# Kernel tuning notes

Hardware: AMD Instinct MI355X
Metric: run time of the kernel (lower is better)

## Reference

```python
import jax, jax.numpy as jnp
import numpy as np

EPS = 1e-6
TEMPERATURE = 0.75
SINKHORN_ITERS = 7


def setup_inputs() -> dict:
    key = jax.random.key(0)
    ks = jax.random.split(key, 6)
    b, h, t, d_h = 4, 8, 4096, 64
    bs = 256
    nb = t // bs
    q = jax.random.normal(ks[0], (b, h, t, d_h), jnp.float32)
    k = jax.random.normal(ks[1], (b, h, t, d_h), jnp.float32)
    v = jax.random.normal(ks[2], (b, h, t, d_h), jnp.float32)
    # uniform noise for gumbel sampling in the sinkhorn sort net
    gumbel_u = jax.random.uniform(ks[3], (b * h, nb, nb), jnp.float32,
                                  minval=EPS, maxval=1.0 - EPS)
    W_out = jax.random.normal(ks[4], (2 * d_h, d_h), jnp.float32) / np.sqrt(2 * d_h)
    b_out = jnp.zeros((d_h,), jnp.float32)
    return {"q": q, "k": k, "v": v, "gumbel_u": gumbel_u,
            "W_out": W_out, "b_out": b_out, "bucket_size": bs}


def _sinkhorn(r, n_iters):
    # iterative row/col log-normalization of log-scores r: [bh, nb, nb]
    def body(r, _):
        r = r - jax.scipy.special.logsumexp(r, axis=2, keepdims=True)
        r = r - jax.scipy.special.logsumexp(r, axis=1, keepdims=True)
        return r, None
    r, _ = jax.lax.scan(body, r, None, length=n_iters)
    return jnp.exp(r)


def reference(q, k, v, gumbel_u, W_out, b_out, bucket_size):
    b, h, t, d_h = q.shape
    bh = b * h
    nb = t // bucket_size
    scale = d_h ** -0.5
    # merge batch/head and bucket: [bh, nb, bs, d_h]
    bq = q.reshape(bh, nb, bucket_size, d_h)
    bk = k.reshape(bh, nb, bucket_size, d_h)
    bv = v.reshape(bh, nb, bucket_size, d_h)
    # AttentionSortNet: bucket sums -> scores -> gumbel sinkhorn soft permutation
    q_sum = bq.sum(axis=2)  # [bh, nb, d_h]
    k_sum = bk.sum(axis=2)
    R0 = jax.nn.relu(jnp.einsum('bie,bje->bij', q_sum, k_sum) * scale)
    gumbel = -jnp.log(-jnp.log(gumbel_u + EPS) + EPS)
    r = (jnp.log(R0 + EPS) + gumbel) / TEMPERATURE
    R = _sinkhorn(r, SINKHORN_ITERS)  # [bh, nb, nb]
    # soft-reorder k/v buckets with R
    k_r = jnp.einsum('bij,bjsd->bisd', R, bk)
    v_r = jnp.einsum('bij,bjsd->bisd', R, bv)
    # local (within-bucket) attention
    local_s = jnp.einsum('bnie,bnje->bnij', bq, bk) * scale
    local_out = jnp.einsum('bnij,bnjd->bnid', jax.nn.softmax(local_s, axis=-1), bv)
    # attention over soft-sorted buckets
    sort_s = jnp.einsum('bnie,bnje->bnij', bq, k_r) * scale
    sort_out = jnp.einsum('bnij,bnjd->bnid', jax.nn.softmax(sort_s, axis=-1), v_r)
    # concat local + sorted heads, project 2*d_h -> d_h
    out = jnp.concatenate([local_out, sort_out], axis=-1)  # [bh, nb, bs, 2*d_h]
    out = out @ W_out + b_out
    return out.reshape(b, h, t, d_h)
```

## Files before the change

### kernel.cpp

```cpp
#include <hip/hip_runtime.h>
#include <math.h>


typedef __attribute__((ext_vector_type(8))) short short8;
typedef __attribute__((ext_vector_type(4))) float f32x4;

constexpr int BH = 32;
constexpr int NB = 16;
constexpr int BS = 256;
constexpr int D  = 64;
constexpr int BUCKET = BS * D;
constexpr float SCALE = 0.125f;

__device__ inline unsigned short bf16_rne(float x) {
  unsigned u = __builtin_bit_cast(unsigned, x);
  unsigned r = u + 0x7FFFu + ((u >> 16) & 1u);
  return (unsigned short)(r >> 16);
}
__device__ inline float bf16_to_f(unsigned short h) {
  unsigned u = ((unsigned)h) << 16;
  return __builtin_bit_cast(float, u);
}
__device__ inline void split2(float x, unsigned short& h, unsigned short& l) {
  h = bf16_rne(x);
  l = bf16_rne(x - bf16_to_f(h));
}
__device__ inline uint2 pack4(unsigned short a, unsigned short b,
                              unsigned short c, unsigned short d) {
  uint2 r;
  r.x = (unsigned)a | ((unsigned)b << 16);
  r.y = (unsigned)c | ((unsigned)d << 16);
  return r;
}

__global__ __launch_bounds__(256) void k_bucket_sums(
    const float* __restrict__ q, const float* __restrict__ k,
    float* __restrict__ qsum, float* __restrict__ ksum) {
  const int bid = blockIdx.x;
  const int t = threadIdx.x;
  const int d = t & 63;
  const int grp = t >> 6;
  const float* qb = q + (size_t)bid * BUCKET;
  const float* kb = k + (size_t)bid * BUCKET;
  float sq = 0.f, sk = 0.f;
  for (int s = grp; s < BS; s += 4) {
    sq += qb[s * D + d];
    sk += kb[s * D + d];
  }
  __shared__ float red[2][4][64];
  red[0][grp][d] = sq;
  red[1][grp][d] = sk;
  __syncthreads();
  if (t < 64) {
    qsum[bid * D + t] = red[0][0][t] + red[0][1][t] + red[0][2][t] + red[0][3][t];
  } else if (t < 128) {
    const int dd = t - 64;
    ksum[bid * D + dd] = red[1][0][dd] + red[1][1][dd] + red[1][2][dd] + red[1][3][dd];
  }
}

__global__ __launch_bounds__(256) void k_sinkhorn(
    const float* __restrict__ qsum, const float* __restrict__ ksum,
    const float* __restrict__ gu, float* __restrict__ R) {
  const int bh = blockIdx.x;
  const int t = threadIdx.x;
  const int i = t >> 4, j = t & 15;
  __shared__ float qs[16][64], ks[16][64], r[16][17];
  for (int idx = t; idx < NB * D; idx += 256) {
    qs[idx >> 6][idx & 63] = qsum[bh * NB * D + idx];
    ks[idx >> 6][idx & 63] = ksum[bh * NB * D + idx];
  }
  __syncthreads();
  float dot = 0.f;
  #pragma unroll
  for (int e = 0; e < D; ++e) dot += qs[i][e] * ks[j][e];
  const float R0 = fmaxf(dot * SCALE, 0.f);
  const float u = gu[bh * 256 + t];
  const float g = -logf(-logf(u + 1e-6f) + 1e-6f);
  float rv = (logf(R0 + 1e-6f) + g) * (1.0f / 0.75f);
  r[i][j] = rv;
  __syncthreads();
  for (int it = 0; it < 7; ++it) {
    float m = -1e30f;
    #pragma unroll
    for (int jj = 0; jj < 16; ++jj) m = fmaxf(m, r[i][jj]);
    float ssum = 0.f;
    #pragma unroll
    for (int jj = 0; jj < 16; ++jj) ssum += expf(r[i][jj] - m);
    float nv = r[i][j] - (m + logf(ssum));
    __syncthreads();
    r[i][j] = nv;
    __syncthreads();
    m = -1e30f;
    #pragma unroll
    for (int ii = 0; ii < 16; ++ii) m = fmaxf(m, r[ii][j]);
    ssum = 0.f;
    #pragma unroll
    for (int ii = 0; ii < 16; ++ii) ssum += expf(r[ii][j] - m);
    nv = r[i][j] - (m + logf(ssum));
    __syncthreads();
    r[i][j] = nv;
    __syncthreads();
  }
  R[bh * 256 + t] = expf(r[i][j]);
}

__global__ __launch_bounds__(256) void k_mix(
    const float* __restrict__ k, const float* __restrict__ v,
    const float* __restrict__ R,
    float* __restrict__ kr, float* __restrict__ vr) {
  const int bid = blockIdx.x;
  const int bh = bid >> 4;
  const int c4 = bid & 15;
  const int t = threadIdx.x;
  __shared__ float Rs[16][16];
  Rs[t >> 4][t & 15] = R[bh * 256 + t];
  __syncthreads();
  const int f = c4 * 256 + t;
  const float4* kb = (const float4*)(k + (size_t)bh * NB * BUCKET);
  const float4* vb = (const float4*)(v + (size_t)bh * NB * BUCKET);
  float4 ka[16], va[16];
  #pragma unroll
  for (int i = 0; i < 16; ++i) {
    ka[i] = make_float4(0.f, 0.f, 0.f, 0.f);
    va[i] = make_float4(0.f, 0.f, 0.f, 0.f);
  }
  #pragma unroll
  for (int j = 0; j < 16; ++j) {
    const float4 kv = kb[j * 4096 + f];
    const float4 vv = vb[j * 4096 + f];
    #pragma unroll
    for (int i = 0; i < 16; ++i) {
      const float w = Rs[i][j];
      ka[i].x += w * kv.x; ka[i].y += w * kv.y; ka[i].z += w * kv.z; ka[i].w += w * kv.w;
      va[i].x += w * vv.x; va[i].y += w * vv.y; va[i].z += w * vv.z; va[i].w += w * vv.w;
    }
  }
  float4* kro = (float4*)(kr + (size_t)bh * NB * BUCKET);
  float4* vro = (float4*)(vr + (size_t)bh * NB * BUCKET);
  #pragma unroll
  for (int i = 0; i < 16; ++i) {
    kro[i * 4096 + f] = ka[i];
    vro[i * 4096 + f] = va[i];
  }
}

__global__ __launch_bounds__(256, 2) void k_attn(
    const float* __restrict__ q,
    const float* __restrict__ k,  const float* __restrict__ v,
    const float* __restrict__ kr, const float* __restrict__ vr,
    const float* __restrict__ Wp, const float* __restrict__ bp,
    float* __restrict__ out) {
  const int bid = blockIdx.x;
  const int t = threadIdx.x;
  const int wv = t >> 6;
  const int lane = t & 63;
  const int g = lane >> 4;
  const int c = lane & 15;
  const size_t boff = (size_t)bid * BUCKET;

  __shared__ unsigned short Khi[32 * 72], Klo[32 * 72];
  __shared__ unsigned short VThi[64 * 40], VTlo[64 * 40];
  __shared__ float Plds[4][64 * 36];

  short8 Qhi[4][2], Qlo[4][2];
  #pragma unroll
  for (int qm = 0; qm < 4; ++qm) {
    #pragma unroll
    for (int ks = 0; ks < 2; ++ks) {
      const float* src = q + boff + (size_t)(64 * wv + 16 * qm + c) * D + 32 * ks + 8 * g;
      float4 a = *(const float4*)src;
      float4 b = *(const float4*)(src + 4);
      float xs[8] = {a.x, a.y, a.z, a.w, b.x, b.y, b.z, b.w};
      short8 hi, lo;
      #pragma unroll
      for (int e = 0; e < 8; ++e) {
        unsigned short h, l2;
        split2(xs[e] * SCALE, h, l2);
        hi[e] = (short)h; lo[e] = (short)l2;
      }
      Qhi[qm][ks] = hi; Qlo[qm][ks] = lo;
    }
  }
  short8 ONE8;
  #pragma unroll
  for (int e = 0; e < 8; ++e) ONE8[e] = (short)0x3F80;

  float* Pw = &Plds[wv][0];

  f32x4 Pacc[4][4];
  #pragma unroll
  for (int qm = 0; qm < 4; ++qm)
    #pragma unroll
    for (int dn = 0; dn < 4; ++dn) Pacc[qm][dn] = (f32x4){0.f, 0.f, 0.f, 0.f};

  #pragma unroll
  for (int pass = 0; pass < 2; ++pass) {
    const float* kb = (pass ? kr : k) + boff;
    const float* vb = (pass ? vr : v) + boff;
    f32x4 Oacc[4][4];
    f32x4 lacc[4];
    #pragma unroll
    for (int qm = 0; qm < 4; ++qm) {
      lacc[qm] = (f32x4){0.f, 0.f, 0.f, 0.f};
      #pragma unroll
      for (int dn = 0; dn < 4; ++dn) Oacc[qm][dn] = (f32x4){0.f, 0.f, 0.f, 0.f};
    }

    for (int p = 0; p < 8; ++p) {
      __syncthreads();
      if (t < 128) {
        #pragma unroll
        for (int i = 0; i < 4; ++i) {
          int cell = t + 128 * i;
          int kkr = cell >> 4, dq = cell & 15;
          float4 a = *(const float4*)(kb + (size_t)(32 * p + kkr) * D + 4 * dq);
          unsigned short h0, l0, h1, l1, h2, l2, h3, l3;
          split2(a.x, h0, l0); split2(a.y, h1, l1);
          split2(a.z, h2, l2); split2(a.w, h3, l3);
          *(uint2*)&Khi[kkr * 72 + 4 * dq] = pack4(h0, h1, h2, h3);
          *(uint2*)&Klo[kkr * 72 + 4 * dq] = pack4(l0, l1, l2, l3);
        }
      } else {
        int h2i = t - 128;
        int kkq = h2i >> 4, dq = h2i & 15;
        float4 rows[4];
        #pragma unroll
        for (int j = 0; j < 4; ++j)
          rows[j] = *(const float4*)(vb + (size_t)(32 * p + 4 * kkq + j) * D + 4 * dq);
        #pragma unroll
        for (int m = 0; m < 4; ++m) {
          float e0 = (m == 0) ? rows[0].x : (m == 1) ? rows[0].y : (m == 2) ? rows[0].z : rows[0].w;
          float e1 = (m == 0) ? rows[1].x : (m == 1) ? rows[1].y : (m == 2) ? rows[1].z : rows[1].w;
          float e2 = (m == 0) ? rows[2].x : (m == 1) ? rows[2].y : (m == 2) ? rows[2].z : rows[2].w;
          float e3 = (m == 0) ? rows[3].x : (m == 1) ? rows[3].y : (m == 2) ? rows[3].z : rows[3].w;
          unsigned short h0, l0, h1, l1, h2, l2, h3, l3;
          split2(e0, h0, l0); split2(e1, h1, l1);
          split2(e2, h2, l2); split2(e3, h3, l3);
          *(uint2*)&VThi[(4 * dq + m) * 40 + 4 * kkq] = pack4(h0, h1, h2, h3);
          *(uint2*)&VTlo[(4 * dq + m) * 40 + 4 * kkq] = pack4(l0, l1, l2, l3);
        }
      }
      __syncthreads();

      #pragma unroll
      for (int kn = 0; kn < 2; ++kn) {
        f32x4 S[4];
        #pragma unroll
        for (int qm = 0; qm < 4; ++qm) S[qm] = (f32x4){0.f, 0.f, 0.f, 0.f};
        #pragma unroll
        for (int ks = 0; ks < 2; ++ks) {
          short8 Bhi = *(const short8*)&Khi[(16 * kn + c) * 72 + 32 * ks + 8 * g];
          short8 Blo = *(const short8*)&Klo[(16 * kn + c) * 72 + 32 * ks + 8 * g];
          #pragma unroll
          for (int qm = 0; qm < 4; ++qm) {
            S[qm] = __builtin_amdgcn_mfma_f32_16x16x32_bf16(Qhi[qm][ks], Bhi, S[qm], 0, 0, 0);
            S[qm] = __builtin_amdgcn_mfma_f32_16x16x32_bf16(Qhi[qm][ks], Blo, S[qm], 0, 0, 0);
            S[qm] = __builtin_amdgcn_mfma_f32_16x16x32_bf16(Qlo[qm][ks], Bhi, S[qm], 0, 0, 0);
          }
        }
        #pragma unroll
        for (int qm = 0; qm < 4; ++qm)
          #pragma unroll
          for (int r = 0; r < 4; ++r)
            Pw[(16 * qm + 4 * g + r) * 36 + 16 * kn + c] = __expf(S[qm][r]);
      }

      short8 Phi[4], Plo[4];
      #pragma unroll
      for (int qm = 0; qm < 4; ++qm) {
        const float* pr = &Pw[(16 * qm + c) * 36 + 8 * g];
        f32x4 p0 = *(const f32x4*)pr;
        f32x4 p1 = *(const f32x4*)(pr + 4);
        float ps[8] = {p0[0], p0[1], p0[2], p0[3], p1[0], p1[1], p1[2], p1[3]};
        short8 hi, lo;
        #pragma unroll
        for (int e = 0; e < 8; ++e) {
          unsigned short h, l2;
          split2(ps[e], h, l2);
          hi[e] = (short)h; lo[e] = (short)l2;
        }
        Phi[qm] = hi; Plo[qm] = lo;
      }

      #pragma unroll
      for (int qm = 0; qm < 4; ++qm) {
        lacc[qm] = __builtin_amdgcn_mfma_f32_16x16x32_bf16(Phi[qm], ONE8, lacc[qm], 0, 0, 0);
        lacc[qm] = __builtin_amdgcn_mfma_f32_16x16x32_bf16(Plo[qm], ONE8, lacc[qm], 0, 0, 0);
      }

      #pragma unroll
      for (int dn = 0; dn < 4; ++dn) {
        short8 Vhi = *(const short8*)&VThi[(16 * dn + c) * 40 + 8 * g];
        short8 Vlo = *(const short8*)&VTlo[(16 * dn + c) * 40 + 8 * g];
        #pragma unroll
        for (int qm = 0; qm < 4; ++qm) {
          Oacc[qm][dn] = __builtin_amdgcn_mfma_f32_16x16x32_bf16(Phi[qm], Vhi, Oacc[qm][dn], 0, 0, 0);
          Oacc[qm][dn] = __builtin_amdgcn_mfma_f32_16x16x32_bf16(Phi[qm], Vlo, Oacc[qm][dn], 0, 0, 0);
          Oacc[qm][dn] = __builtin_amdgcn_mfma_f32_16x16x32_bf16(Plo[qm], Vhi, Oacc[qm][dn], 0, 0, 0);
        }
      }
    }

    f32x4 invs[4];
    #pragma unroll
    for (int qm = 0; qm < 4; ++qm)
      #pragma unroll
      for (int r = 0; r < 4; ++r) invs[qm][r] = 1.0f / lacc[qm][r];

    #pragma unroll
    for (int ks2 = 0; ks2 < 2; ++ks2) {
      #pragma unroll
      for (int qm = 0; qm < 4; ++qm)
        #pragma unroll
        for (int dnl = 0; dnl < 2; ++dnl) {
          const int dn = 2 * ks2 + dnl;
          #pragma unroll
          for (int r = 0; r < 4; ++r)
            Pw[(16 * qm + 4 * g + r) * 36 + 16 * dnl + c] = Oacc[qm][dn][r] * invs[qm][r];
        }
      short8 Ahi[4], Alo[4];
      #pragma unroll
      for (int qm = 0; qm < 4; ++qm) {
        const float* pr = &Pw[(16 * qm + c) * 36 + 8 * g];
        f32x4 p0 = *(const f32x4*)pr;
        f32x4 p1 = *(const f32x4*)(pr + 4);
        float ps[8] = {p0[0], p0[1], p0[2], p0[3], p1[0], p1[1], p1[2], p1[3]};
        short8 hi, lo;
        #pragma unroll
        for (int e = 0; e < 8; ++e) {
          unsigned short h, l2;
          split2(ps[e], h, l2);
          hi[e] = (short)h; lo[e] = (short)l2;
        }
        Ahi[qm] = hi; Alo[qm] = lo;
      }
      #pragma unroll
      for (int dn_o = 0; dn_o < 4; ++dn_o) {
        float wf[8];
        #pragma unroll
        for (int e = 0; e < 8; ++e)
          wf[e] = Wp[(size_t)(pass * 64 + 32 * ks2 + 8 * g + e) * 64 + 16 * dn_o + c];
        short8 WBhi, WBlo;
        #pragma unroll
        for (int e = 0; e < 8; ++e) {
          unsigned short h, l2;
          split2(wf[e], h, l2);
          WBhi[e] = (short)h; WBlo[e] = (short)l2;
        }
        #pragma unroll
        for (int qm = 0; qm < 4; ++qm) {
          Pacc[qm][dn_o] = __builtin_amdgcn_mfma_f32_16x16x32_bf16(Ahi[qm], WBhi, Pacc[qm][dn_o], 0, 0, 0);
          Pacc[qm][dn_o] = __builtin_amdgcn_mfma_f32_16x16x32_bf16(Ahi[qm], WBlo, Pacc[qm][dn_o], 0, 0, 0);
          Pacc[qm][dn_o] = __builtin_amdgcn_mfma_f32_16x16x32_bf16(Alo[qm], WBhi, Pacc[qm][dn_o], 0, 0, 0);
        }
      }
    }
  }

  float bvals[4];
  #pragma unroll
  for (int dn_o = 0; dn_o < 4; ++dn_o) bvals[dn_o] = bp[16 * dn_o + c];
  #pragma unroll
  for (int qm = 0; qm < 4; ++qm)
    #pragma unroll
    for (int dn_o = 0; dn_o < 4; ++dn_o)
      #pragma unroll
      for (int r = 0; r < 4; ++r) {
        const int row = 64 * wv + 16 * qm + 4 * g + r;
        out[((size_t)bid * 256 + row) * 64 + 16 * dn_o + c] = Pacc[qm][dn_o][r] + bvals[dn_o];
      }
}

extern "C" void kernel_launch(void* const* d_in, const int* in_sizes, int n_in,
                              void* d_out, int out_size, void* d_ws, size_t ws_size,
                              hipStream_t stream) {
  (void)in_sizes; (void)n_in; (void)out_size; (void)ws_size;
  const float* q  = (const float*)d_in[0];
  const float* k  = (const float*)d_in[1];
  const float* v  = (const float*)d_in[2];
  const float* gu = (const float*)d_in[3];
  const float* W  = (const float*)d_in[4];
  const float* b  = (const float*)d_in[5];
  float* out = (float*)d_out;

  float* ws   = (float*)d_ws;
  float* R    = ws;
  float* qsum = ws + 8192;
  float* ksum = qsum + 32768;
  float* kr   = ksum + 32768;
  float* vr   = kr + 8388608;

  hipLaunchKernelGGL(k_bucket_sums, dim3(BH * NB), dim3(256), 0, stream, q, k, qsum, ksum);
  hipLaunchKernelGGL(k_sinkhorn,    dim3(BH),      dim3(256), 0, stream, qsum, ksum, gu, R);
  hipLaunchKernelGGL(k_mix,         dim3(BH * NB), dim3(256), 0, stream, k, v, R, kr, vr);
  hipLaunchKernelGGL(k_attn,        dim3(BH * NB), dim3(256), 0, stream,
                     q, k, v, kr, vr, W, b, out);
}
```

Baseline: 283.4 us.

## Compute S transposed, keep P in registers, shrink LDS, raise occupancy

Several changes at once. The attention kernel computes S transposed (K as the A operand), so exponentiated scores stay in registers. Row sums come from register adds plus wave shuffles instead of MFMA-with-ones, and P and the normalized output are staged in LDS as packed bf16 hi/lo rather than fp32. The bf16 split is vectorized into pair packing, and the kernel's launch-bound occupancy target goes from 2 to 4. Separately, the bucket-sum kernel now uses float4 loads, and the mix kernel uses float2 with twice as many blocks and fewer registers. The risk is register spilling under the tighter launch bound and a slightly different summation order for the normalizer.

Result: slower. 513.7 us (+81.3%).

```diff
diff --git a/kernel.cpp b/kernel.cpp
--- a/kernel.cpp
+++ b/kernel.cpp
@@ -12,25 +12,18 @@
 constexpr int BUCKET = BS * D;
 constexpr float SCALE = 0.125f;
 
-__device__ inline unsigned short bf16_rne(float x) {
+__device__ inline unsigned bf16_rne_u(float x) {
   unsigned u = __builtin_bit_cast(unsigned, x);
-  unsigned r = u + 0x7FFFu + ((u >> 16) & 1u);
-  return (unsigned short)(r >> 16);
-}
-__device__ inline float bf16_to_f(unsigned short h) {
-  unsigned u = ((unsigned)h) << 16;
-  return __builtin_bit_cast(float, u);
-}
-__device__ inline void split2(float x, unsigned short& h, unsigned short& l) {
-  h = bf16_rne(x);
-  l = bf16_rne(x - bf16_to_f(h));
-}
-__device__ inline uint2 pack4(unsigned short a, unsigned short b,
-                              unsigned short c, unsigned short d) {
-  uint2 r;
-  r.x = (unsigned)a | ((unsigned)b << 16);
-  r.y = (unsigned)c | ((unsigned)d << 16);
-  return r;
+  return (u + 0x7FFFu + ((u >> 16) & 1u)) >> 16;
+}
+__device__ inline unsigned cvt2_bf16(float a, float b) {
+  return bf16_rne_u(a) | (bf16_rne_u(b) << 16);
+}
+__device__ inline void split_pair(float a, float b, unsigned& uhi, unsigned& ulo) {
+  uhi = cvt2_bf16(a, b);
+  float ha = __builtin_bit_cast(float, uhi << 16);
+  float hb = __builtin_bit_cast(float, uhi & 0xFFFF0000u);
+  ulo = cvt2_bf16(a - ha, b - hb);
 }
 
 __global__ __launch_bounds__(256) void k_bucket_sums(
@@ -38,24 +31,29 @@
     float* __restrict__ qsum, float* __restrict__ ksum) {
   const int bid = blockIdx.x;
   const int t = threadIdx.x;
-  const int d = t & 63;
-  const int grp = t >> 6;
-  const float* qb = q + (size_t)bid * BUCKET;
-  const float* kb = k + (size_t)bid * BUCKET;
-  float sq = 0.f, sk = 0.f;
-  for (int s = grp; s < BS; s += 4) {
-    sq += qb[s * D + d];
-    sk += kb[s * D + d];
-  }
-  __shared__ float red[2][4][64];
-  red[0][grp][d] = sq;
-  red[1][grp][d] = sk;
+  const int c4 = t & 15;
+  const int rg = t >> 4;
+  const float4* qb = (const float4*)(q + (size_t)bid * BUCKET);
+  const float4* kb = (const float4*)(k + (size_t)bid * BUCKET);
+  float4 sq = make_float4(0.f, 0.f, 0.f, 0.f);
+  float4 sk = make_float4(0.f, 0.f, 0.f, 0.f);
+  for (int s = rg; s < BS; s += 16) {
+    float4 a = qb[s * 16 + c4];
+    float4 b2 = kb[s * 16 + c4];
+    sq.x += a.x; sq.y += a.y; sq.z += a.z; sq.w += a.w;
+    sk.x += b2.x; sk.y += b2.y; sk.z += b2.z; sk.w += b2.w;
+  }
+  __shared__ float red[2][16][64];
+  *(float4*)&red[0][rg][4 * c4] = sq;
+  *(float4*)&red[1][rg][4 * c4] = sk;
   __syncthreads();
-  if (t < 64) {
-    qsum[bid * D + t] = red[0][0][t] + red[0][1][t] + red[0][2][t] + red[0][3][t];
-  } else if (t < 128) {
-    const int dd = t - 64;
-    ksum[bid * D + dd] = red[1][0][dd] + red[1][1][dd] + red[1][2][dd] + red[1][3][dd];
+  if (t < 128) {
+    const int which = t >> 6;
+    const int d = t & 63;
+    float s = 0.f;
+    #pragma unroll
+    for (int g2 = 0; g2 < 16; ++g2) s += red[which][g2][d];
+    (which ? ksum : qsum)[bid * D + d] = s;
   }
 }
 
@@ -105,47 +103,47 @@
   R[bh * 256 + t] = expf(r[i][j]);
 }
 
-__global__ __launch_bounds__(256) void k_mix(
+__global__ __launch_bounds__(256, 4) void k_mix(
     const float* __restrict__ k, const float* __restrict__ v,
     const float* __restrict__ R,
     float* __restrict__ kr, float* __restrict__ vr) {
   const int bid = blockIdx.x;
-  const int bh = bid >> 4;
-  const int c4 = bid & 15;
+  const int bh = bid >> 5;
+  const int ch = bid & 31;
   const int t = threadIdx.x;
   __shared__ float Rs[16][16];
   Rs[t >> 4][t & 15] = R[bh * 256 + t];
   __syncthreads();
-  const int f = c4 * 256 + t;
-  const float4* kb = (const float4*)(k + (size_t)bh * NB * BUCKET);
-  const float4* vb = (const float4*)(v + (size_t)bh * NB * BUCKET);
-  float4 ka[16], va[16];
+  const int f = ch * 256 + t;
+  const float2* kb = (const float2*)(k + (size_t)bh * NB * BUCKET);
+  const float2* vb = (const float2*)(v + (size_t)bh * NB * BUCKET);
+  float2 ka[16], va[16];
   #pragma unroll
   for (int i = 0; i < 16; ++i) {
-    ka[i] = make_float4(0.f, 0.f, 0.f, 0.f);
-    va[i] = make_float4(0.f, 0.f, 0.f, 0.f);
+    ka[i] = make_float2(0.f, 0.f);
+    va[i] = make_float2(0.f, 0.f);
   }
   #pragma unroll
   for (int j = 0; j < 16; ++j) {
-    const float4 kv = kb[j * 4096 + f];
-    const float4 vv = vb[j * 4096 + f];
+    const float2 kv = kb[j * 8192 + f];
+    const float2 vv = vb[j * 8192 + f];
     #pragma unroll
     for (int i = 0; i < 16; ++i) {
       const float w = Rs[i][j];
-      ka[i].x += w * kv.x; ka[i].y += w * kv.y; ka[i].z += w * kv.z; ka[i].w += w * kv.w;
-      va[i].x += w * vv.x; va[i].y += w * vv.y; va[i].z += w * vv.z; va[i].w += w * vv.w;
-    }
-  }
-  float4* kro = (float4*)(kr + (size_t)bh * NB * BUCKET);
-  float4* vro = (float4*)(vr + (size_t)bh * NB * BUCKET);
+      ka[i].x += w * kv.x; ka[i].y += w * kv.y;
+      va[i].x += w * vv.x; va[i].y += w * vv.y;
+    }
+  }
+  float2* kro = (float2*)(kr + (size_t)bh * NB * BUCKET);
+  float2* vro = (float2*)(vr + (size_t)bh * NB * BUCKET);
   #pragma unroll
   for (int i = 0; i < 16; ++i) {
-    kro[i * 4096 + f] = ka[i];
-    vro[i * 4096 + f] = va[i];
-  }
-}
-
-__global__ __launch_bounds__(256, 2) void k_attn(
+    kro[i * 8192 + f] = ka[i];
+    vro[i * 8192 + f] = va[i];
+  }
+}
+
+__global__ __launch_bounds__(256, 4) void k_attn(
     const float* __restrict__ q,
     const float* __restrict__ k,  const float* __restrict__ v,
     const float* __restrict__ kr, const float* __restrict__ vr,
@@ -161,7 +159,7 @@
 
   __shared__ unsigned short Khi[32 * 72], Klo[32 * 72];
   __shared__ unsigned short VThi[64 * 40], VTlo[64 * 40];
-  __shared__ float Plds[4][64 * 36];
+  __shared__ unsigned short Pbh[4][16 * 40], Pbl[4][16 * 40];
 
   short8 Qhi[4][2], Qlo[4][2];
   #pragma unroll
@@ -170,23 +168,21 @@
     for (int ks = 0; ks < 2; ++ks) {
       const float* src = q + boff + (size_t)(64 * wv + 16 * qm + c) * D + 32 * ks + 8 * g;
       float4 a = *(const float4*)src;
-      float4 b = *(const float4*)(src + 4);
-      float xs[8] = {a.x, a.y, a.z, a.w, b.x, b.y, b.z, b.w};
-      short8 hi, lo;
-      #pragma unroll
-      for (int e = 0; e < 8; ++e) {
-        unsigned short h, l2;
-        split2(xs[e] * SCALE, h, l2);
-        hi[e] = (short)h; lo[e] = (short)l2;
-      }
-      Qhi[qm][ks] = hi; Qlo[qm][ks] = lo;
-    }
-  }
-  short8 ONE8;
-  #pragma unroll
-  for (int e = 0; e < 8; ++e) ONE8[e] = (short)0x3F80;
-
-  float* Pw = &Plds[wv][0];
+      float4 b2 = *(const float4*)(src + 4);
+      unsigned h0, l0, h1, l1, h2, l2, h3, l3;
+      split_pair(a.x * SCALE, a.y * SCALE, h0, l0);
+      split_pair(a.z * SCALE, a.w * SCALE, h1, l1);
+      split_pair(b2.x * SCALE, b2.y * SCALE, h2, l2);
+      split_pair(b2.z * SCALE, b2.w * SCALE, h3, l3);
+      uint4 uh = make_uint4(h0, h1, h2, h3);
+      uint4 ul = make_uint4(l0, l1, l2, l3);
+      Qhi[qm][ks] = __builtin_bit_cast(short8, uh);
+      Qlo[qm][ks] = __builtin_bit_cast(short8, ul);
+    }
+  }
+
+  unsigned short* ph = Pbh[wv];
+  unsigned short* pl = Pbl[wv];
 
   f32x4 Pacc[4][4];
   #pragma unroll
@@ -199,10 +195,10 @@
     const float* kb = (pass ? kr : k) + boff;
     const float* vb = (pass ? vr : v) + boff;
     f32x4 Oacc[4][4];
-    f32x4 lacc[4];
+    float lrow[4];
     #pragma unroll
     for (int qm = 0; qm < 4; ++qm) {
-      lacc[qm] = (f32x4){0.f, 0.f, 0.f, 0.f};
+      lrow[qm] = 0.f;
       #pragma unroll
       for (int dn = 0; dn < 4; ++dn) Oacc[qm][dn] = (f32x4){0.f, 0.f, 0.f, 0.f};
     }
@@ -215,11 +211,11 @@
           int cell = t + 128 * i;
           int kkr = cell >> 4, dq = cell & 15;
           float4 a = *(const float4*)(kb + (size_t)(32 * p + kkr) * D + 4 * dq);
-          unsigned short h0, l0, h1, l1, h2, l2, h3, l3;
-          split2(a.x, h0, l0); split2(a.y, h1, l1);
-          split2(a.z, h2, l2); split2(a.w, h3, l3);
-          *(uint2*)&Khi[kkr * 72 + 4 * dq] = pack4(h0, h1, h2, h3);
-          *(uint2*)&Klo[kkr * 72 + 4 * dq] = pack4(l0, l1, l2, l3);
+          unsigned h0, l0, h1, l1;
+          split_pair(a.x, a.y, h0, l0);
+          split_pair(a.z, a.w, h1, l1);
+          *(uint2*)&Khi[kkr * 72 + 4 * dq] = make_uint2(h0, h1);
+          *(uint2*)&Klo[kkr * 72 + 4 * dq] = make_uint2(l0, l1);
         }
       } else {
         int h2i = t - 128;
@@ -234,59 +230,57 @@
           float e1 = (m == 0) ? rows[1].x : (m == 1) ? rows[1].y : (m == 2) ? rows[1].z : rows[1].w;
           float e2 = (m == 0) ? rows[2].x : (m == 1) ? rows[2].y : (m == 2) ? rows[2].z : rows[2].w;
           float e3 = (m == 0) ? rows[3].x : (m == 1) ? rows[3].y : (m == 2) ? rows[3].z : rows[3].w;
-          unsigned short h0, l0, h1, l1, h2, l2, h3, l3;
-          split2(e0, h0, l0); split2(e1, h1, l1);
-          split2(e2, h2, l2); split2(e3, h3, l3);
-          *(uint2*)&VThi[(4 * dq + m) * 40 + 4 * kkq] = pack4(h0, h1, h2, h3);
-          *(uint2*)&VTlo[(4 * dq + m) * 40 + 4 * kkq] = pack4(l0, l1, l2, l3);
+          unsigned h0, l0, h1, l1;
+          split_pair(e0, e1, h0, l0);
+          split_pair(e2, e3, h1, l1);
+          *(uint2*)&VThi[(4 * dq + m) * 40 + 4 * kkq] = make_uint2(h0, h1);
+          *(uint2*)&VTlo[(4 * dq + m) * 40 + 4 * kkq] = make_uint2(l0, l1);
         }
       }
       __syncthreads();
 
+      f32x4 pe[4][2];
       #pragma unroll
       for (int kn = 0; kn < 2; ++kn) {
-        f32x4 S[4];
-        #pragma unroll
-        for (int qm = 0; qm < 4; ++qm) S[qm] = (f32x4){0.f, 0.f, 0.f, 0.f};
+        f32x4 ST[4];
+        #pragma unroll
+        for (int qm = 0; qm < 4; ++qm) ST[qm] = (f32x4){0.f, 0.f, 0.f, 0.f};
         #pragma unroll
         for (int ks = 0; ks < 2; ++ks) {
-          short8 Bhi = *(const short8*)&Khi[(16 * kn + c) * 72 + 32 * ks + 8 * g];
-          short8 Blo = *(const short8*)&Klo[(16 * kn + c) * 72 + 32 * ks + 8 * g];
+          short8 KAhi = *(const short8*)&Khi[(16 * kn + c) * 72 + 32 * ks + 8 * g];
+          short8 KAlo = *(const short8*)&Klo[(16 * kn + c) * 72 + 32 * ks + 8 * g];
           #pragma unroll
           for (int qm = 0; qm < 4; ++qm) {
-            S[qm] = __builtin_amdgcn_mfma_f32_16x16x32_bf16(Qhi[qm][ks], Bhi, S[qm], 0, 0, 0);
-            S[qm] = __builtin_amdgcn_mfma_f32_16x16x32_bf16(Qhi[qm][ks], Blo, S[qm], 0, 0, 0);
-            S[qm] = __builtin_amdgcn_mfma_f32_16x16x32_bf16(Qlo[qm][ks], Bhi, S[qm], 0, 0, 0);
+            ST[qm] = __builtin_amdgcn_mfma_f32_16x16x32_bf16(KAhi, Qhi[qm][ks], ST[qm], 0, 0, 0);
+            ST[qm] = __builtin_amdgcn_mfma_f32_16x16x32_bf16(KAhi, Qlo[qm][ks], ST[qm], 0, 0, 0);
+            ST[qm] = __builtin_amdgcn_mfma_f32_16x16x32_bf16(KAlo, Qhi[qm][ks], ST[qm], 0, 0, 0);
           }
         }
         #pragma unroll
         for (int qm = 0; qm < 4; ++qm)
           #pragma unroll
-          for (int r = 0; r < 4; ++r)
-            Pw[(16 * qm + 4 * g + r) * 36 + 16 * kn + c] = __expf(S[qm][r]);
+          for (int r = 0; r < 4; ++r) pe[qm][kn][r] = __expf(ST[qm][r]);
+      }
+
+      #pragma unroll
+      for (int qm = 0; qm < 4; ++qm) {
+        lrow[qm] += ((pe[qm][0][0] + pe[qm][0][1]) + (pe[qm][0][2] + pe[qm][0][3]))
+                  + ((pe[qm][1][0] + pe[qm][1][1]) + (pe[qm][1][2] + pe[qm][1][3]));
       }
 
       short8 Phi[4], Plo[4];
       #pragma unroll
       for (int qm = 0; qm < 4; ++qm) {
-        const float* pr = &Pw[(16 * qm + c) * 36 + 8 * g];
-        f32x4 p0 = *(const f32x4*)pr;
-        f32x4 p1 = *(const f32x4*)(pr + 4);
-        float ps[8] = {p0[0], p0[1], p0[2], p0[3], p1[0], p1[1], p1[2], p1[3]};
-        short8 hi, lo;
-        #pragma unroll
-        for (int e = 0; e < 8; ++e) {
-          unsigned short h, l2;
-          split2(ps[e], h, l2);
-          hi[e] = (short)h; lo[e] = (short)l2;
-        }
-        Phi[qm] = hi; Plo[qm] = lo;
-      }
-
-      #pragma unroll
-      for (int qm = 0; qm < 4; ++qm) {
-        lacc[qm] = __builtin_amdgcn_mfma_f32_16x16x32_bf16(Phi[qm], ONE8, lacc[qm], 0, 0, 0);
-        lacc[qm] = __builtin_amdgcn_mfma_f32_16x16x32_bf16(Plo[qm], ONE8, lacc[qm], 0, 0, 0);
+        #pragma unroll
+        for (int kn = 0; kn < 2; ++kn) {
+          unsigned h0, l0, h1, l1;
+          split_pair(pe[qm][kn][0], pe[qm][kn][1], h0, l0);
+          split_pair(pe[qm][kn][2], pe[qm][kn][3], h1, l1);
+          *(uint2*)&ph[c * 40 + 16 * kn + 4 * g] = make_uint2(h0, h1);
+          *(uint2*)&pl[c * 40 + 16 * kn + 4 * g] = make_uint2(l0, l1);
+        }
+        Phi[qm] = *(const short8*)&ph[c * 40 + 8 * g];
+        Plo[qm] = *(const short8*)&pl[c * 40 + 8 * g];
       }
 
       #pragma unroll
@@ -304,36 +298,37 @@
 
     f32x4 invs[4];
     #pragma unroll
-    for (int qm = 0; qm < 4; ++qm)
-      #pragma unroll
-      for (int r = 0; r < 4; ++r) invs[qm][r] = 1.0f / lacc[qm][r];
+    for (int qm = 0; qm < 4; ++qm) {
+      float s = lrow[qm];
+      s += __shfl_xor(s, 16, 64);
+      s += __shfl_xor(s, 32, 64);
+      #pragma unroll
+      for (int r = 0; r < 4; ++r) invs[qm][r] = 1.0f / __shfl(s, 4 * g + r, 64);
+    }
 
     #pragma unroll
     for (int ks2 = 0; ks2 < 2; ++ks2) {
-      #pragma unroll
-      for (int qm = 0; qm < 4; ++qm)
+      short8 Ahi[4], Alo[4];
+      #pragma unroll
+      for (int qm = 0; qm < 4; ++qm) {
         #pragma unroll
         for (int dnl = 0; dnl < 2; ++dnl) {
           const int dn = 2 * ks2 + dnl;
-          #pragma unroll
-          for (int r = 0; r < 4; ++r)
-            Pw[(16 * qm + 4 * g + r) * 36 + 16 * dnl + c] = Oacc[qm][dn][r] * invs[qm][r];
-        }
-      short8 Ahi[4], Alo[4];
-      #pragma unroll
-      for (int qm = 0; qm < 4; ++qm) {
-        const float* pr = &Pw[(16 * qm + c) * 36 + 8 * g];
-        f32x4 p0 = *(const f32x4*)pr;
-        f32x4 p1 = *(const f32x4*)(pr + 4);
-        float ps[8] = {p0[0], p0[1], p0[2], p0[3], p1[0], p1[1], p1[2], p1[3]};
-        short8 hi, lo;
-        #pragma unroll
-        for (int e = 0; e < 8; ++e) {
-          unsigned short h, l2;
-          split2(ps[e], h, l2);
-          hi[e] = (short)h; lo[e] = (short)l2;
-        }
-        Ahi[qm] = hi; Alo[qm] = lo;
+          unsigned uh0, ul0, uh1, ul1;
+          split_pair(Oacc[qm][dn][0] * invs[qm][0], Oacc[qm][dn][1] * invs[qm][1], uh0, ul0);
+          split_pair(Oacc[qm][dn][2] * invs[qm][2], Oacc[qm][dn][3] * invs[qm][3], uh1, ul1);
+          const int base = 16 * dnl + c;
+          ph[(4 * g + 0) * 40 + base] = (unsigned short)(uh0 & 0xFFFFu);
+          ph[(4 * g + 1) * 40 + base] = (unsigned short)(uh0 >> 16);
+          ph[(4 * g + 2) * 40 + base] = (unsigned short)(uh1 & 0xFFFFu);
+          ph[(4 * g + 3) * 40 + base] = (unsigned short)(uh1 >> 16);
+          pl[(4 * g + 0) * 40 + base] = (unsigned short)(ul0 & 0xFFFFu);
+          pl[(4 * g + 1) * 40 + base] = (unsigned short)(ul0 >> 16);
+          pl[(4 * g + 2) * 40 + base] = (unsigned short)(ul1 & 0xFFFFu);
+          pl[(4 * g + 3) * 40 + base] = (unsigned short)(ul1 >> 16);
+        }
+        Ahi[qm] = *(const short8*)&ph[c * 40 + 8 * g];
+        Alo[qm] = *(const short8*)&pl[c * 40 + 8 * g];
       }
       #pragma unroll
       for (int dn_o = 0; dn_o < 4; ++dn_o) {
@@ -341,13 +336,15 @@
         #pragma unroll
         for (int e = 0; e < 8; ++e)
           wf[e] = Wp[(size_t)(pass * 64 + 32 * ks2 + 8 * g + e) * 64 + 16 * dn_o + c];
-        short8 WBhi, WBlo;
-        #pragma unroll
-        for (int e = 0; e < 8; ++e) {
-          unsigned short h, l2;
-          split2(wf[e], h, l2);
-          WBhi[e] = (short)h; WBlo[e] = (short)l2;
-        }
+        unsigned h0, l0, h1, l1, h2, l2, h3, l3;
+        split_pair(wf[0], wf[1], h0, l0);
+        split_pair(wf[2], wf[3], h1, l1);
+        split_pair(wf[4], wf[5], h2, l2);
+        split_pair(wf[6], wf[7], h3, l3);
+        uint4 uh = make_uint4(h0, h1, h2, h3);
+        uint4 ul = make_uint4(l0, l1, l2, l3);
+        short8 WBhi = __builtin_bit_cast(short8, uh);
+        short8 WBlo = __builtin_bit_cast(short8, ul);
         #pragma unroll
         for (int qm = 0; qm < 4; ++qm) {
           Pacc[qm][dn_o] = __builtin_amdgcn_mfma_f32_16x16x32_bf16(Ahi[qm], WBhi, Pacc[qm][dn_o], 0, 0, 0);
@@ -393,7 +390,7 @@
 
   hipLaunchKernelGGL(k_bucket_sums, dim3(BH * NB), dim3(256), 0, stream, q, k, qsum, ksum);
   hipLaunchKernelGGL(k_sinkhorn,    dim3(BH),      dim3(256), 0, stream, qsum, ksum, gu, R);
-  hipLaunchKernelGGL(k_mix,         dim3(BH * NB), dim3(256), 0, stream, k, v, R, kr, vr);
+  hipLaunchKernelGGL(k_mix,         dim3(BH * 32), dim3(256), 0, stream, k, v, R, kr, vr);
   hipLaunchKernelGGL(k_attn,        dim3(BH * NB), dim3(256), 0, stream,
                      q, k, v, kr, vr, W, b, out);
 }
```
